# Kernel tuning notes

Measured on AMD Instinct MI355X. Metric: run time of the kernel, lower is better.

## Reference

```python
import jax, jax.numpy as jnp
import numpy as np

M, N, K = 1024, 11008, 4096


def _unpack_i2u(Bp):
    """Unpack 2-bit unsigned weights per decode_i2u_to_i8s interleave.

    Bp: [N, K//4] int8 storage. Within each group of 4 bytes (16 elements),
    output element at position 4*i + j = (byte_j >> (2*i)) & 3.
    Returns [N, K] int8 with values in {0,1,2,3}.
    """
    Bu = jax.lax.bitcast_convert_type(Bp, jnp.uint8)  # [N, K//4]
    n, kc = Bu.shape
    Bg = Bu.reshape(n, kc // 4, 1, 4)                 # [N, G, 1, j]
    shifts = (jnp.arange(4, dtype=jnp.uint8) * jnp.uint8(2)).reshape(1, 1, 4, 1)
    vals = (Bg >> shifts) & jnp.uint8(3)              # [N, G, i, j]
    return vals.reshape(n, kc * 4).astype(jnp.int8)   # [N, K]


def setup_inputs() -> dict:
    key = jax.random.key(0)
    k1, k2 = jax.random.split(key)
    A = jax.random.randint(k1, (M, K), -128, 128, dtype=jnp.int8)
    B = jax.random.randint(k2, (N, K // 4), -128, 128, dtype=jnp.int8)
    return {"A": A, "B": B}


def reference(A, B):
    W = _unpack_i2u(B)  # [N, K] int8
    C = jax.lax.dot_general(
        A, W,
        dimension_numbers=(((1,), (1,)), ((), ())),
        preferred_element_type=jnp.int32,
    )  # [M, N] int32
    return C
```

## Files before the change

### kernel.cpp

```cpp
#include <hip/hip_runtime.h>
#include <stdint.h>


#define MM 1024
#define NN 11008
#define KK 4096
#define KSTEPS 64
#define MTILES (MM / 128)
#define NTILES (NN / 128)
#define NBLOCKS (16 * NTILES)

using i32x4  = __attribute__((ext_vector_type(4))) int;
using i32x16 = __attribute__((ext_vector_type(16))) int;

__device__ __forceinline__ int pack4(i32x4 v) {
    return (int)(((uint32_t)v[0] & 0xFFu) | (((uint32_t)v[1] & 0xFFu) << 8)
               | (((uint32_t)v[2] & 0xFFu) << 16) | (((uint32_t)v[3] & 0xFFu) << 24));
}

__global__ __launch_bounds__(256) void prep_A(const int* __restrict__ src,
                                              uint8_t* __restrict__ dst) {
    const int g = blockIdx.x * 256 + threadIdx.x;
    const int kstep = g >> 12;
    const int rem   = g & 4095;
    const int mtile = rem >> 9;
    const int c     = rem & 511;
    const int row32 = (c >> 7) & 3, kk2 = (c >> 6) & 1;
    const int lane  = c & 63;
    const int row   = mtile * 128 + row32 * 32 + (lane & 31);
    const int kbyte = kstep * 64 + kk2 * 32 + (lane >> 5) * 16;
    const i32x4* s4 = (const i32x4*)(src + (size_t)row * KK + kbyte);
    i32x4 o;
#pragma unroll
    for (int q = 0; q < 4; ++q) o[q] = pack4(s4[q]);
    *(i32x4*)(dst + (size_t)g * 16) = o;
}

__global__ __launch_bounds__(256) void prep_B(const int* __restrict__ src,
                                              uint8_t* __restrict__ dst) {
    const int t = blockIdx.x * 256 + threadIdx.x;
    const int n = t >> 6, kstep = t & 63;
    const int ntile = n >> 7, wc = (n >> 6) & 1, ni = (n >> 5) & 1, l31 = n & 31;
    const i32x4* s4 = (const i32x4*)(src + (size_t)n * (KK / 4) + kstep * 16);
    int w[4];
#pragma unroll
    for (int j = 0; j < 4; ++j) w[j] = pack4(s4[j]);
    uint8_t* base = dst + ((size_t)kstep * NTILES + ntile) * 2048 + wc * 1024;
    *(int2*)(base + l31 * 16 + ni * 8)        = make_int2(w[0], w[2]);
    *(int2*)(base + (l31 + 32) * 16 + ni * 8) = make_int2(w[1], w[3]);
}

struct Bfrag { i32x4 c0, c1; };

__global__ __launch_bounds__(128, 2) void bitnet_gemm(const uint8_t* __restrict__ A2,
                                                      const uint8_t* __restrict__ B3,
                                                      int* __restrict__ C) {
    const int tid  = threadIdx.x;
    const int lane = tid & 63, wid = tid >> 6;
    const int l31  = lane & 31, h = lane >> 5;

    const int bid = blockIdx.x;
    const int l   = (bid & 7) * (NBLOCKS / 8) + (bid >> 3);
    const int wm  = l & 15;
    const int wn  = l >> 4;
    const int mtile = wm >> 1, half = wm & 1;

    const size_t strideA = (size_t)MTILES * 8192;
    const size_t strideB = (size_t)NTILES * 2048;
    const int ksbase = wid * (KSTEPS / 2);

    const uint8_t* pa[4];
#pragma unroll
    for (int s = 0; s < 4; ++s) {
        const int mi = s >> 1, kk2 = s & 1;
        pa[s] = A2 + (size_t)ksbase * strideA + (size_t)mtile * 8192
              + ((half * 2 + mi) * 2 + kk2) * 1024 + lane * 16;
    }
    const uint8_t* pb = B3 + (size_t)ksbase * strideB + (size_t)wn * 2048 + lane * 16;

    i32x16 acc[2][4] = {};
    i32x4 fa0[4], fa1[4];
    Bfrag fp0, fp1;

    auto LOAD = [&](i32x4 (&a)[4], Bfrag& p, int ks) {
#pragma unroll
        for (int s = 0; s < 4; ++s)
            a[s] = *(const i32x4*)(pa[s] + (size_t)ks * strideA);
        p.c0 = *(const i32x4*)(pb + (size_t)ks * strideB);
        p.c1 = *(const i32x4*)(pb + (size_t)ks * strideB + 1024);
    };

    auto COMPUTE = [&](const i32x4 (&a)[4], const Bfrag& p) {
#pragma unroll
        for (int kk2 = 0; kk2 < 2; ++kk2) {
#pragma unroll
            for (int nc = 0; nc < 4; ++nc) {
                const uint32_t q = (uint32_t)((nc < 2 ? p.c0 : p.c1)[(nc & 1) * 2 + kk2]);
                i32x4 b;
#pragma unroll
                for (int i = 0; i < 4; ++i)
                    b[i] = (int)((q >> (2 * i)) & 0x03030303u);
                acc[0][nc] = __builtin_amdgcn_mfma_i32_32x32x32_i8(a[0 + kk2], b, acc[0][nc], 0, 0, 0);
                acc[1][nc] = __builtin_amdgcn_mfma_i32_32x32x32_i8(a[2 + kk2], b, acc[1][nc], 0, 0, 0);
            }
        }
    };

    LOAD(fa0, fp0, 0);
    LOAD(fa1, fp1, 1);

#pragma unroll 1
    for (int ks = 0; ks < KSTEPS / 2 - 2; ks += 2) {
        COMPUTE(fa0, fp0); LOAD(fa0, fp0, ks + 2);
        COMPUTE(fa1, fp1); LOAD(fa1, fp1, ks + 3);
    }
    COMPUTE(fa0, fp0);
    COMPUTE(fa1, fp1);

    __shared__ __align__(16) i32x4 red[8 * 4 * 64];
    if (wid == 1) {
#pragma unroll
        for (int mi = 0; mi < 2; ++mi)
#pragma unroll
            for (int nc = 0; nc < 4; ++nc) {
                const i32x16 v = acc[mi][nc];
#pragma unroll
                for (int q = 0; q < 4; ++q) {
                    i32x4 s;
                    s[0] = v[q * 4 + 0]; s[1] = v[q * 4 + 1];
                    s[2] = v[q * 4 + 2]; s[3] = v[q * 4 + 3];
                    red[((mi * 4 + nc) * 4 + q) * 64 + lane] = s;
                }
            }
    }
    __syncthreads();
    if (wid == 0) {
        const int brow = wm * 64, bcol = wn * 128;
#pragma unroll
        for (int mi = 0; mi < 2; ++mi)
#pragma unroll
            for (int nc = 0; nc < 4; ++nc) {
                i32x16 v = acc[mi][nc];
#pragma unroll
                for (int q = 0; q < 4; ++q) {
                    const i32x4 r = red[((mi * 4 + nc) * 4 + q) * 64 + lane];
                    v[q * 4 + 0] += r[0]; v[q * 4 + 1] += r[1];
                    v[q * 4 + 2] += r[2]; v[q * 4 + 3] += r[3];
                }
                const int colg = bcol + nc * 32 + l31;
#pragma unroll
                for (int r = 0; r < 16; ++r) {
                    const int rowin = (r & 3) + 8 * (r >> 2) + 4 * h;
                    const int rowg  = brow + mi * 32 + rowin;
                    C[(size_t)rowg * NN + colg] = v[r];
                }
            }
    }
}

extern "C" void kernel_launch(void* const* d_in, const int* in_sizes, int n_in,
                              void* d_out, int out_size, void* d_ws, size_t ws_size,
                              hipStream_t stream) {
    const int* A32 = (const int*)d_in[0];
    const int* B32 = (const int*)d_in[1];
    int* C = (int*)d_out;

    uint8_t* A2 = (uint8_t*)d_ws;
    uint8_t* B3 = A2 + (size_t)MM * KK;

    prep_A<<<dim3((MM * KK / 16) / 256), dim3(256), 0, stream>>>(A32, A2);
    prep_B<<<dim3((NN * 64) / 256), dim3(256), 0, stream>>>(B32, B3);
    bitnet_gemm<<<dim3(NBLOCKS), dim3(128), 0, stream>>>(A2, B3, C);
}
```

Before: 73.51 us.

## Stage A tiles via direct global-to-LDS loads with deep pipeline and merge prep kernels

```diff
diff --git a/kernel.cpp b/kernel.cpp
--- a/kernel.cpp
+++ b/kernel.cpp
@@ -5,10 +5,11 @@
 #define MM 1024
 #define NN 11008
 #define KK 4096
-#define KSTEPS 64
-#define MTILES (MM / 128)
-#define NTILES (NN / 128)
+#define MTILES 8
+#define NTILES 86
 #define NBLOCKS (16 * NTILES)
+#define STRIDE_A ((size_t)MTILES * 8192)
+#define STRIDE_B ((size_t)NTILES * 2048)
 
 using i32x4  = __attribute__((ext_vector_type(4))) int;
 using i32x16 = __attribute__((ext_vector_type(16))) int;
@@ -18,39 +19,101 @@
                | (((uint32_t)v[2] & 0xFFu) << 16) | (((uint32_t)v[3] & 0xFFu) << 24));
 }
 
-__global__ __launch_bounds__(256) void prep_A(const int* __restrict__ src,
-                                              uint8_t* __restrict__ dst) {
-    const int g = blockIdx.x * 256 + threadIdx.x;
-    const int kstep = g >> 12;
-    const int rem   = g & 4095;
-    const int mtile = rem >> 9;
-    const int c     = rem & 511;
-    const int row32 = (c >> 7) & 3, kk2 = (c >> 6) & 1;
-    const int lane  = c & 63;
-    const int row   = mtile * 128 + row32 * 32 + (lane & 31);
-    const int kbyte = kstep * 64 + kk2 * 32 + (lane >> 5) * 16;
-    const i32x4* s4 = (const i32x4*)(src + (size_t)row * KK + kbyte);
-    i32x4 o;
-#pragma unroll
-    for (int q = 0; q < 4; ++q) o[q] = pack4(s4[q]);
-    *(i32x4*)(dst + (size_t)g * 16) = o;
-}
-
-__global__ __launch_bounds__(256) void prep_B(const int* __restrict__ src,
-                                              uint8_t* __restrict__ dst) {
-    const int t = blockIdx.x * 256 + threadIdx.x;
-    const int n = t >> 6, kstep = t & 63;
-    const int ntile = n >> 7, wc = (n >> 6) & 1, ni = (n >> 5) & 1, l31 = n & 31;
-    const i32x4* s4 = (const i32x4*)(src + (size_t)n * (KK / 4) + kstep * 16);
-    int w[4];
-#pragma unroll
-    for (int j = 0; j < 4; ++j) w[j] = pack4(s4[j]);
-    uint8_t* base = dst + ((size_t)kstep * NTILES + ntile) * 2048 + wc * 1024;
-    *(int2*)(base + l31 * 16 + ni * 8)        = make_int2(w[0], w[2]);
-    *(int2*)(base + (l31 + 32) * 16 + ni * 8) = make_int2(w[1], w[3]);
-}
-
-struct Bfrag { i32x4 c0, c1; };
+__global__ __launch_bounds__(256) void prep_AB(const int* __restrict__ Asrc,
+                                               const int* __restrict__ Bsrc,
+                                               uint8_t* __restrict__ A2,
+                                               uint8_t* __restrict__ B3) {
+    if (blockIdx.x < 1024) {
+        const int g = blockIdx.x * 256 + threadIdx.x;
+        const int kstep = g >> 12;
+        const int rem   = g & 4095;
+        const int mtile = rem >> 9;
+        const int c     = rem & 511;
+        const int row32 = (c >> 7) & 3, kk2 = (c >> 6) & 1;
+        const int lane  = c & 63;
+        const int row   = mtile * 128 + row32 * 32 + (lane & 31);
+        const int kbyte = kstep * 64 + kk2 * 32 + (lane >> 5) * 16;
+        const i32x4* s4 = (const i32x4*)(Asrc + (size_t)row * KK + kbyte);
+        i32x4 o;
+#pragma unroll
+        for (int q = 0; q < 4; ++q) o[q] = pack4(s4[q]);
+        *(i32x4*)(A2 + (size_t)g * 16) = o;
+    } else {
+        const int t = (blockIdx.x - 1024) * 256 + threadIdx.x;
+        const int n = t >> 6, kstep = t & 63;
+        const int ntile = n >> 7, hf = (n >> 6) & 1, ni = (n >> 5) & 1, l31 = n & 31;
+        const i32x4* s4 = (const i32x4*)(Bsrc + (size_t)n * (KK / 4) + kstep * 16);
+        int w[4];
+#pragma unroll
+        for (int j = 0; j < 4; ++j) w[j] = pack4(s4[j]);
+        uint8_t* base = B3 + ((size_t)kstep * NTILES + ntile) * 2048 + hf * 1024;
+        *(int2*)(base + l31 * 16 + ni * 8)        = make_int2(w[0], w[2]);
+        *(int2*)(base + (l31 + 32) * 16 + ni * 8) = make_int2(w[1], w[3]);
+    }
+}
+
+#define GLOAD_LDS16(g, l) __builtin_amdgcn_global_load_lds(                    \
+        (const __attribute__((address_space(1))) uint32_t*)(g),                \
+        (__attribute__((address_space(3))) uint32_t*)(l), 16, 0, 0)
+
+#define MFMA_I8 __builtin_amdgcn_mfma_i32_32x32x32_i8
+
+#define STAGE(T) do {                                                          \
+    const uint8_t* at_ = gA + (size_t)((T) + 3) * STRIDE_A;                    \
+    uint8_t* ls_ = &As[wid][((T) + 3) & 3][0];                                 \
+    GLOAD_LDS16(at_,        ls_);                                              \
+    GLOAD_LDS16(at_ + 1024, ls_ + 1024);                                       \
+    GLOAD_LDS16(at_ + 2048, ls_ + 2048);                                       \
+    GLOAD_LDS16(at_ + 3072, ls_ + 3072);                                       \
+} while (0)
+
+#define BLOAD(BI, T) do {                                                      \
+    c0[BI] = *(const i32x4*)(gB + (size_t)(T) * STRIDE_B);                     \
+    c1[BI] = *(const i32x4*)(gB + (size_t)(T) * STRIDE_B + 1024);              \
+} while (0)
+
+#define COMP(T, BI) do {                                                       \
+    const uint8_t* ab_ = &As[wid][(T) & 3][0];                                 \
+    i32x4 a00 = *(const i32x4*)(ab_ + lane * 16);                              \
+    i32x4 a01 = *(const i32x4*)(ab_ + 1024 + lane * 16);                       \
+    i32x4 a10 = *(const i32x4*)(ab_ + 2048 + lane * 16);                       \
+    i32x4 a11 = *(const i32x4*)(ab_ + 3072 + lane * 16);                       \
+    _Pragma("unroll")                                                          \
+    for (int kk2_ = 0; kk2_ < 2; ++kk2_) {                                     \
+        const uint32_t q0_ = (uint32_t)c0[BI][kk2_];                           \
+        const uint32_t q1_ = (uint32_t)c0[BI][2 + kk2_];                       \
+        const uint32_t q2_ = (uint32_t)c1[BI][kk2_];                           \
+        const uint32_t q3_ = (uint32_t)c1[BI][2 + kk2_];                       \
+        i32x4 b0_, b1_, b2_, b3_;                                              \
+        _Pragma("unroll")                                                      \
+        for (int i_ = 0; i_ < 4; ++i_) {                                       \
+            b0_[i_] = (int)((q0_ >> (2 * i_)) & 0x03030303u);                  \
+            b1_[i_] = (int)((q1_ >> (2 * i_)) & 0x03030303u);                  \
+            b2_[i_] = (int)((q2_ >> (2 * i_)) & 0x03030303u);                  \
+            b3_[i_] = (int)((q3_ >> (2 * i_)) & 0x03030303u);                  \
+        }                                                                      \
+        const i32x4 am0_ = kk2_ ? a01 : a00;                                   \
+        const i32x4 am1_ = kk2_ ? a11 : a10;                                   \
+        __builtin_amdgcn_s_setprio(1);                                         \
+        acc[0][0] = MFMA_I8(am0_, b0_, acc[0][0], 0, 0, 0);                    \
+        acc[0][1] = MFMA_I8(am0_, b1_, acc[0][1], 0, 0, 0);                    \
+        acc[0][2] = MFMA_I8(am0_, b2_, acc[0][2], 0, 0, 0);                    \
+        acc[0][3] = MFMA_I8(am0_, b3_, acc[0][3], 0, 0, 0);                    \
+        acc[1][0] = MFMA_I8(am1_, b0_, acc[1][0], 0, 0, 0);                    \
+        acc[1][1] = MFMA_I8(am1_, b1_, acc[1][1], 0, 0, 0);                    \
+        acc[1][2] = MFMA_I8(am1_, b2_, acc[1][2], 0, 0, 0);                    \
+        acc[1][3] = MFMA_I8(am1_, b3_, acc[1][3], 0, 0, 0);                    \
+        __builtin_amdgcn_s_setprio(0);                                         \
+    }                                                                          \
+} while (0)
+
+#define ITER(T, BCUR, BNXT, NW, DOSTAGE, DOB) do {                             \
+    if (DOSTAGE) STAGE(T);                                                     \
+    if (DOB)     BLOAD(BNXT, (T) + 2);                                         \
+    asm volatile("s_waitcnt vmcnt(" #NW ")" ::: "memory");                     \
+    __builtin_amdgcn_sched_barrier(0);                                         \
+    COMP(T, BCUR);                                                             \
+} while (0)
 
 __global__ __launch_bounds__(128, 2) void bitnet_gemm(const uint8_t* __restrict__ A2,
                                                       const uint8_t* __restrict__ B3,
@@ -63,61 +126,32 @@
     const int l   = (bid & 7) * (NBLOCKS / 8) + (bid >> 3);
     const int wm  = l & 15;
     const int wn  = l >> 4;
-    const int mtile = wm >> 1, half = wm & 1;
-
-    const size_t strideA = (size_t)MTILES * 8192;
-    const size_t strideB = (size_t)NTILES * 2048;
-    const int ksbase = wid * (KSTEPS / 2);
-
-    const uint8_t* pa[4];
-#pragma unroll
-    for (int s = 0; s < 4; ++s) {
-        const int mi = s >> 1, kk2 = s & 1;
-        pa[s] = A2 + (size_t)ksbase * strideA + (size_t)mtile * 8192
-              + ((half * 2 + mi) * 2 + kk2) * 1024 + lane * 16;
-    }
-    const uint8_t* pb = B3 + (size_t)ksbase * strideB + (size_t)wn * 2048 + lane * 16;
+
+    __shared__ __align__(16) uint8_t As[2][4][4096];
+
+    const uint8_t* gA = A2 + (size_t)(wid * 32) * STRIDE_A + wm * 4096 + lane * 16;
+    const uint8_t* gB = B3 + (size_t)(wid * 32) * STRIDE_B + (size_t)wn * 2048 + lane * 16;
 
     i32x16 acc[2][4] = {};
-    i32x4 fa0[4], fa1[4];
-    Bfrag fp0, fp1;
-
-    auto LOAD = [&](i32x4 (&a)[4], Bfrag& p, int ks) {
-#pragma unroll
-        for (int s = 0; s < 4; ++s)
-            a[s] = *(const i32x4*)(pa[s] + (size_t)ks * strideA);
-        p.c0 = *(const i32x4*)(pb + (size_t)ks * strideB);
-        p.c1 = *(const i32x4*)(pb + (size_t)ks * strideB + 1024);
-    };
-
-    auto COMPUTE = [&](const i32x4 (&a)[4], const Bfrag& p) {
-#pragma unroll
-        for (int kk2 = 0; kk2 < 2; ++kk2) {
-#pragma unroll
-            for (int nc = 0; nc < 4; ++nc) {
-                const uint32_t q = (uint32_t)((nc < 2 ? p.c0 : p.c1)[(nc & 1) * 2 + kk2]);
-                i32x4 b;
-#pragma unroll
-                for (int i = 0; i < 4; ++i)
-                    b[i] = (int)((q >> (2 * i)) & 0x03030303u);
-                acc[0][nc] = __builtin_amdgcn_mfma_i32_32x32x32_i8(a[0 + kk2], b, acc[0][nc], 0, 0, 0);
-                acc[1][nc] = __builtin_amdgcn_mfma_i32_32x32x32_i8(a[2 + kk2], b, acc[1][nc], 0, 0, 0);
-            }
-        }
-    };
-
-    LOAD(fa0, fp0, 0);
-    LOAD(fa1, fp1, 1);
-
+    i32x4 c0[3], c1[3];
+
+    STAGE(-3); STAGE(-2); STAGE(-1);
+    BLOAD(0, 0); BLOAD(1, 1);
+
+    ITER(0, 0, 2, 8, 1, 1);
+    ITER(1, 1, 0, 8, 1, 1);
 #pragma unroll 1
-    for (int ks = 0; ks < KSTEPS / 2 - 2; ks += 2) {
-        COMPUTE(fa0, fp0); LOAD(fa0, fp0, ks + 2);
-        COMPUTE(fa1, fp1); LOAD(fa1, fp1, ks + 3);
-    }
-    COMPUTE(fa0, fp0);
-    COMPUTE(fa1, fp1);
-
-    __shared__ __align__(16) i32x4 red[8 * 4 * 64];
+    for (int t = 2; t < 29; t += 3) {
+        ITER(t,     2, 1, 12, 1, 1);
+        ITER(t + 1, 0, 2, 12, 1, 1);
+        ITER(t + 2, 1, 0, 12, 1, 1);
+    }
+    ITER(29, 2, 1, 8, 0, 1);
+    ITER(30, 0, 0, 2, 0, 0);
+    ITER(31, 1, 0, 0, 0, 0);
+
+    __syncthreads();
+    i32x4* red = (i32x4*)&As[0][0][0];
     if (wid == 1) {
 #pragma unroll
         for (int mi = 0; mi < 2; ++mi)
@@ -168,7 +202,6 @@
     uint8_t* A2 = (uint8_t*)d_ws;
     uint8_t* B3 = A2 + (size_t)MM * KK;
 
-    prep_A<<<dim3((MM * KK / 16) / 256), dim3(256), 0, stream>>>(A32, A2);
-    prep_B<<<dim3((NN * 64) / 256), dim3(256), 0, stream>>>(B32, B3);
+    prep_AB<<<dim3(1024 + 2752), dim3(256), 0, stream>>>(A32, B32, A2, B3);
     bitnet_gemm<<<dim3(NBLOCKS), dim3(128), 0, stream>>>(A2, B3, C);
 }
```

Measured after the change: 78.32 us. 1.07x slower.
